# Kernel tuning notes

Measured on AMD Instinct MI355X. Metric: run time of the kernel, lower is better.

## Reference

```python
import jax, jax.numpy as jnp
import numpy as np

N = 40000   # nodes
E = 320000  # edges (avg degree 8)
H = 32      # hidden_dim
V = 128     # in_dim_node (node feature vocab)
EPS = 1e-5  # BatchNorm eps


def setup_inputs() -> dict:
    key = jax.random.key(0)
    ks = jax.random.split(key, 14)
    s = 0.05
    return {
        "h": jax.random.normal(ks[0], (N, H), jnp.float32),
        "e": jax.random.normal(ks[1], (E, H), jnp.float32),  # unused by forward (overwritten), kept for signature fidelity
        "feat": jax.random.randint(ks[2], (N,), 0, V),
        "src_idx": jax.random.randint(ks[3], (E,), 0, N),
        "dst_idx": jax.random.randint(ks[4], (E,), 0, N),
        "emb_src": jax.random.normal(ks[5], (V, H), jnp.float32) * s,
        "emb_dst": jax.random.normal(ks[6], (V, H), jnp.float32) * s,
        "W_edge": jax.random.normal(ks[7], (2 * H, H), jnp.float32) * s,
        "b_edge": jnp.zeros((H,), jnp.float32),
        "W1": jax.random.normal(ks[8], (H, H * H), jnp.float32) * s,  # proj1: H -> H^2
        "b1": jnp.zeros((H * H,), jnp.float32),
        "W2": jax.random.normal(ks[9], (H, H), jnp.float32) * s,      # proj2: H -> H
        "b2": jnp.zeros((H,), jnp.float32),
        "W3": jax.random.normal(ks[10], (H, H), jnp.float32) * s,     # edge_proj3
        "b3": jnp.zeros((H,), jnp.float32),
        "gamma": jnp.ones((H,), jnp.float32),
        "beta": jnp.zeros((H,), jnp.float32),
    }


def reference(h, e, feat, src_idx, dst_idx, emb_src, emb_dst, W_edge, b_edge,
              W1, b1, W2, b2, W3, b3, gamma, beta):
    # local edge term: embeddings of the integer node features at edge endpoints
    src = emb_src[feat[src_idx]]                      # [E, H]
    dst = emb_dst[feat[dst_idx]]                      # [E, H]
    lr_e_local = jnp.concatenate([src, dst], axis=-1) @ W_edge + b_edge  # [E, H]

    # global low-rank bilinear term. Original builds a dense [N, N, H] tensor
    # (mm of [N*H, H] with [H, N]) and gathers E rows; mathematically
    # out[e, k] = proj1(h[src_e]).reshape(H, H)[k, :] . proj2(h[dst_e]).
    # We compute only the E needed per-edge matvecs.
    P1 = (h @ W1 + b1).reshape(N, H, H)               # [N, H, H]
    P2 = h @ W2 + b2                                  # [N, H]
    lr_e_global = jnp.einsum('ekd,ed->ek', P1[src_idx], P2[dst_idx])  # [E, H]
    lr_e_global = lr_e_global @ W3 + b3

    out = lr_e_local + lr_e_global                    # [E, H]

    # BatchNorm1d over the edge batch (training-mode batch statistics, biased var)
    mean = jnp.mean(out, axis=0)
    var = jnp.mean(jnp.square(out - mean), axis=0)
    out = (out - mean) * jax.lax.rsqrt(var + EPS) * gamma + beta

    # ReLU; dropout omitted (deterministic eval-mode reference)
    return jax.nn.relu(out)
```

## Files before the change

kernel.cpp:

```cpp
#include <hip/hip_runtime.h>

#define N_NODES 40000
#define N_EDGES 320000
#define EPSBN 1e-5f

typedef float floatx4 __attribute__((ext_vector_type(4)));

__global__ void k_setup(const float* __restrict__ W1, float* __restrict__ w1t) {
  int i = blockIdx.x * 256 + threadIdx.x;
  int col = i >> 5, j = i & 31;
  w1t[col * 32 + j] = W1[j * 1024 + col];
}

__global__ void k_p2(const float* __restrict__ h, const float* __restrict__ W2,
                     const float* __restrict__ b2, float* __restrict__ P2) {
  __shared__ float w2s[1024];
  int t = threadIdx.x;
  for (int i = t; i < 1024; i += 256) w2s[i] = W2[i];
  __syncthreads();
  int nl = t >> 5, m = t & 31;
  int n = blockIdx.x * 8 + nl;
  const float* hrow = h + n * 32;
  float a = b2[m];
  #pragma unroll
  for (int j = 0; j < 32; ++j) a = fmaf(hrow[j], w2s[j * 32 + m], a);
  P2[n * 32 + m] = a;
}

__global__ __launch_bounds__(256) void k_edge(
    const float* __restrict__ h, const int* __restrict__ feat,
    const int* __restrict__ src_idx, const int* __restrict__ dst_idx,
    const float* __restrict__ emb_src, const float* __restrict__ emb_dst,
    const float* __restrict__ W_edge, const float* __restrict__ b_edge,
    const float* __restrict__ b1, const float* __restrict__ W3,
    const float* __restrict__ b3, const float* __restrict__ w1t,
    const float* __restrict__ P2, float* __restrict__ out,
    float* __restrict__ bn_acc) {
  __shared__ float red[4][64];
  const int t = threadIdx.x;
  const int e = blockIdx.x * 256 + t;
  const int si = src_idx[e], di = dst_idx[e];
  const int fs = feat[si], fd = feat[di];

  float p2r[32];
  #pragma unroll
  for (int d = 0; d < 32; ++d) p2r[d] = P2[di * 32 + d];

  float vout[32];
  #pragma unroll
  for (int m = 0; m < 32; ++m) vout[m] = b_edge[m] + b3[m];

  #pragma unroll
  for (int j = 0; j < 32; ++j) {
    float ej = emb_src[fs * 32 + j];
    #pragma unroll
    for (int m = 0; m < 32; ++m) vout[m] = fmaf(ej, W_edge[j * 32 + m], vout[m]);
  }
  #pragma unroll
  for (int j = 0; j < 32; ++j) {
    float ej = emb_dst[fd * 32 + j];
    #pragma unroll
    for (int m = 0; m < 32; ++m) vout[m] = fmaf(ej, W_edge[(32 + j) * 32 + m], vout[m]);
  }

  float hs[32];
  #pragma unroll
  for (int j = 0; j < 32; ++j) hs[j] = h[si * 32 + j];

  for (int k = 0; k < 32; ++k) {
    float gk = 0.f;
    #pragma unroll
    for (int d = 0; d < 32; ++d) {
      const float* w1c = w1t + (k * 32 + d) * 32;
      float tmp = b1[k * 32 + d];
      #pragma unroll
      for (int j = 0; j < 32; ++j) tmp = fmaf(hs[j], w1c[j], tmp);
      gk = fmaf(tmp, p2r[d], gk);
    }
    #pragma unroll
    for (int m = 0; m < 32; ++m) vout[m] = fmaf(gk, W3[k * 32 + m], vout[m]);
  }

  #pragma unroll
  for (int m = 0; m < 32; ++m) out[e * 32 + m] = vout[m];

  const int lane = t & 63, wv = t >> 6;
  #pragma unroll
  for (int m = 0; m < 32; ++m) {
    float a = vout[m];
    float b = vout[m] * vout[m];
    #pragma unroll
    for (int off = 1; off < 64; off <<= 1) {
      a += __shfl_xor(a, off);
      b += __shfl_xor(b, off);
    }
    if (lane == 0) { red[wv][m] = a; red[wv][32 + m] = b; }
  }
  __syncthreads();
  if (t < 64) {
    float acc = red[0][t] + red[1][t] + red[2][t] + red[3][t];
    atomicAdd(&bn_acc[t], acc);
  }
}

__global__ void k_bnfin(const float* __restrict__ bn, const float* __restrict__ gamma,
                        const float* __restrict__ beta, float* __restrict__ osc) {
  int m = threadIdx.x;
  float mean = bn[m] / (float)N_EDGES;
  float var = fmaxf(bn[32 + m] / (float)N_EDGES - mean * mean, 0.f);
  float sc = gamma[m] * rsqrtf(var + EPSBN);
  osc[m] = sc;
  osc[32 + m] = beta[m] - mean * sc;
}

__global__ void k_norm(float* __restrict__ out, const float* __restrict__ sc) {
  __shared__ float s[64];
  if (threadIdx.x < 64) s[threadIdx.x] = sc[threadIdx.x];
  __syncthreads();
  const int total = N_EDGES * 32 / 4;
  for (int i = blockIdx.x * blockDim.x + threadIdx.x; i < total; i += gridDim.x * blockDim.x) {
    floatx4 v = ((floatx4*)out)[i];
    int mb = (i * 4) & 31;
    floatx4 r;
    #pragma unroll
    for (int cc = 0; cc < 4; ++cc)
      r[cc] = fmaxf(fmaf(v[cc], s[mb + cc], s[32 + mb + cc]), 0.f);
    ((floatx4*)out)[i] = r;
  }
}

extern "C" void kernel_launch(void* const* d_in, const int* in_sizes, int n_in,
                              void* d_out, int out_size, void* d_ws, size_t ws_size,
                              hipStream_t stream) {
  const float* h       = (const float*)d_in[0];
  const int*   feat    = (const int*)d_in[2];
  const int*   srci    = (const int*)d_in[3];
  const int*   dsti    = (const int*)d_in[4];
  const float* emb_src = (const float*)d_in[5];
  const float* emb_dst = (const float*)d_in[6];
  const float* W_edge  = (const float*)d_in[7];
  const float* b_edge  = (const float*)d_in[8];
  const float* W1      = (const float*)d_in[9];
  const float* b1      = (const float*)d_in[10];
  const float* W2      = (const float*)d_in[11];
  const float* b2      = (const float*)d_in[12];
  const float* W3      = (const float*)d_in[13];
  const float* b3      = (const float*)d_in[14];
  const float* gamma   = (const float*)d_in[15];
  const float* beta    = (const float*)d_in[16];
  float* out = (float*)d_out;
  char* ws = (char*)d_ws;

  float* bn   = (float*)(ws + 0);
  float* osc  = (float*)(ws + 256);
  float* w1t  = (float*)(ws + 512);
  float* P2   = (float*)(ws + 512 + 131072);
  if (ws_size < (size_t)(512 + 131072 + 5120000)) return;

  hipMemsetAsync(bn, 0, 256, stream);
  k_setup<<<128, 256, 0, stream>>>(W1, w1t);
  k_p2<<<N_NODES / 8, 256, 0, stream>>>(h, W2, b2, P2);
  k_edge<<<N_EDGES / 256, 256, 0, stream>>>(h, feat, srci, dsti, emb_src, emb_dst,
                                            W_edge, b_edge, b1, W3, b3, w1t, P2, out, bn);
  k_bnfin<<<1, 32, 0, stream>>>(bn, gamma, beta, osc);
  k_norm<<<2048, 256, 0, stream>>>(out, osc);
}
```

Measured before the change: 877.8 us.

## Use fp16 MFMA for per-edge bilinear term and precompute embedding tables

The per-edge W1 projection of h[src] now runs on 16x16x32 fp16 MFMA with W1 and W3 staged in shared memory, in a persistent grid that handles 128 edges per iteration. The local edge term is folded into per-vocab lookup tables (Tsrc, Tdst), and the b1 bias contribution is folded into a per-node P2c precomputed alongside P2. Together these remove most of the scalar FMA work and the repeated weight reads from global memory per edge. The cost is fp16 rounding of h, W1 and W3, plus an extra N×H workspace buffer.

```diff
diff --git a/kernel.cpp b/kernel.cpp
--- a/kernel.cpp
+++ b/kernel.cpp
@@ -5,18 +5,67 @@
 #define EPSBN 1e-5f
 
 typedef float floatx4 __attribute__((ext_vector_type(4)));
-
-__global__ void k_setup(const float* __restrict__ W1, float* __restrict__ w1t) {
-  int i = blockIdx.x * 256 + threadIdx.x;
-  int col = i >> 5, j = i & 31;
-  w1t[col * 32 + j] = W1[j * 1024 + col];
+typedef _Float16 f16x8 __attribute__((ext_vector_type(8)));
+
+__device__ inline floatx4 mfma16(f16x8 a, f16x8 b, floatx4 c) {
+  return __builtin_amdgcn_mfma_f32_16x16x32_f16(a, b, c, 0, 0, 0);
+}
+
+__device__ inline f16x8 cvt8(floatx4 a, floatx4 b) {
+  f16x8 r;
+  r[0]=(_Float16)a[0]; r[1]=(_Float16)a[1]; r[2]=(_Float16)a[2]; r[3]=(_Float16)a[3];
+  r[4]=(_Float16)b[0]; r[5]=(_Float16)b[1]; r[6]=(_Float16)b[2]; r[7]=(_Float16)b[3];
+  return r;
+}
+
+__global__ void k_pre(const float* __restrict__ W1, const float* __restrict__ b1,
+                      const float* __restrict__ W3, const float* __restrict__ W_edge,
+                      const float* __restrict__ b_edge, const float* __restrict__ b3,
+                      const float* __restrict__ emb_src, const float* __restrict__ emb_dst,
+                      unsigned short* __restrict__ w1t, float* __restrict__ Tsrc,
+                      float* __restrict__ Tdst, unsigned short* __restrict__ w3h,
+                      float* __restrict__ BB) {
+  int t = threadIdx.x, bid = blockIdx.x;
+  if (bid < 128) {
+    int i = bid * 256 + t;
+    int q = i >> 5, j = i & 31;
+    w1t[i] = (unsigned short)__builtin_bit_cast(unsigned short, (_Float16)W1[j * 1024 + q]);
+  } else if (bid < 144) {
+    int i = (bid - 128) * 256 + t;
+    int v = i >> 5, m = i & 31;
+    float a = b_edge[m] + b3[m];
+    #pragma unroll
+    for (int j = 0; j < 32; ++j) a = fmaf(emb_src[v * 32 + j], W_edge[j * 32 + m], a);
+    Tsrc[i] = a;
+  } else if (bid < 160) {
+    int i = (bid - 144) * 256 + t;
+    int v = i >> 5, m = i & 31;
+    float a = 0.f;
+    #pragma unroll
+    for (int j = 0; j < 32; ++j) a = fmaf(emb_dst[v * 32 + j], W_edge[(32 + j) * 32 + m], a);
+    Tdst[i] = a;
+  } else if (bid == 160) {
+    #pragma unroll
+    for (int i = 0; i < 4; ++i) {
+      int idx = t * 4 + i;
+      w3h[idx] = (unsigned short)__builtin_bit_cast(unsigned short, (_Float16)W3[idx]);
+    }
+  } else {
+    int i = (bid - 161) * 256 + t;
+    int d = i >> 5, m = i & 31;
+    float a = 0.f;
+    #pragma unroll
+    for (int k = 0; k < 32; ++k) a = fmaf(b1[k * 32 + d], W3[k * 32 + m], a);
+    BB[i] = a;
+  }
 }
 
 __global__ void k_p2(const float* __restrict__ h, const float* __restrict__ W2,
-                     const float* __restrict__ b2, float* __restrict__ P2) {
-  __shared__ float w2s[1024];
+                     const float* __restrict__ b2, const float* __restrict__ BB,
+                     float* __restrict__ P2, float* __restrict__ P2c) {
+  __shared__ float w2s[1024], bbs[1024], p2l[8][32];
   int t = threadIdx.x;
-  for (int i = t; i < 1024; i += 256) w2s[i] = W2[i];
+  for (int i = t; i < 1024; i += 256) { w2s[i] = W2[i]; bbs[i] = BB[i]; }
   __syncthreads();
   int nl = t >> 5, m = t & 31;
   int n = blockIdx.x * 8 + nl;
@@ -25,80 +74,110 @@
   #pragma unroll
   for (int j = 0; j < 32; ++j) a = fmaf(hrow[j], w2s[j * 32 + m], a);
   P2[n * 32 + m] = a;
-}
-
-__global__ __launch_bounds__(256) void k_edge(
+  p2l[nl][m] = a;
+  __syncthreads();
+  float cacc = 0.f;
+  #pragma unroll
+  for (int d = 0; d < 32; ++d) cacc = fmaf(p2l[nl][d], bbs[d * 32 + m], cacc);
+  P2c[n * 32 + m] = cacc;
+}
+
+__global__ __launch_bounds__(512, 4) void k_edge(
     const float* __restrict__ h, const int* __restrict__ feat,
     const int* __restrict__ src_idx, const int* __restrict__ dst_idx,
-    const float* __restrict__ emb_src, const float* __restrict__ emb_dst,
-    const float* __restrict__ W_edge, const float* __restrict__ b_edge,
-    const float* __restrict__ b1, const float* __restrict__ W3,
-    const float* __restrict__ b3, const float* __restrict__ w1t,
-    const float* __restrict__ P2, float* __restrict__ out,
-    float* __restrict__ bn_acc) {
-  __shared__ float red[4][64];
+    const unsigned short* __restrict__ w1t, const unsigned short* __restrict__ w3h,
+    const float* __restrict__ Tsrc, const float* __restrict__ Tdst,
+    const float* __restrict__ P2, const float* __restrict__ P2c,
+    float* __restrict__ out, float* __restrict__ bn_acc) {
+  __shared__ unsigned short w1l[32768];
+  __shared__ unsigned short w3l[1024];
+  __shared__ float red[8][64];
   const int t = threadIdx.x;
-  const int e = blockIdx.x * 256 + t;
-  const int si = src_idx[e], di = dst_idx[e];
-  const int fs = feat[si], fd = feat[di];
-
-  float p2r[32];
+  for (int i = t; i < 4096; i += 512)
+    ((floatx4*)w1l)[i] = ((const floatx4*)w1t)[i];
+  if (t < 128) ((floatx4*)w3l)[t] = ((const floatx4*)w3h)[t];
+
+  const int lane = t & 63;
+  const int wv = t >> 6;
+  const int c = lane & 15;
+  const int g4 = lane >> 4;
+
+  float s8[8] = {0,0,0,0,0,0,0,0}, q8[8] = {0,0,0,0,0,0,0,0};
+
+  __syncthreads();
+
+  const unsigned short* awp = w1l + c * 32 + g4 * 8;
+  const unsigned short* w3p = w3l + g4 * 8;
+
+  for (int grp = blockIdx.x; grp < N_EDGES / 128; grp += gridDim.x) {
+    const int e = grp * 128 + wv * 16 + c;
+    const int si = src_idx[e];
+    const int di = dst_idx[e];
+    const int fs = feat[si];
+    const int fd = feat[di];
+
+    const floatx4* hp = (const floatx4*)(h + si * 32 + g4 * 8);
+    f16x8 bh = cvt8(hp[0], hp[1]);
+    const floatx4* pp = (const floatx4*)(P2 + di * 32);
+    floatx4 p2a = pp[g4];
+    floatx4 p2b = pp[g4 + 4];
+
+    float v8[8] = {0,0,0,0,0,0,0,0};
+    #pragma unroll
+    for (int k = 0; k < 32; ++k) {
+      f16x8 aw0 = *(const f16x8*)(awp + k * 1024);
+      f16x8 aw1 = *(const f16x8*)(awp + k * 1024 + 512);
+      floatx4 z = {0.f, 0.f, 0.f, 0.f};
+      floatx4 m0 = mfma16(aw0, bh, z);
+      floatx4 m1 = mfma16(aw1, bh, z);
+      float ps = m0[0] * p2a[0];
+      ps = fmaf(m0[1], p2a[1], ps);
+      ps = fmaf(m0[2], p2a[2], ps);
+      ps = fmaf(m0[3], p2a[3], ps);
+      ps = fmaf(m1[0], p2b[0], ps);
+      ps = fmaf(m1[1], p2b[1], ps);
+      ps = fmaf(m1[2], p2b[2], ps);
+      ps = fmaf(m1[3], p2b[3], ps);
+      ps += __shfl_xor(ps, 16);
+      ps += __shfl_xor(ps, 32);
+      const f16x8 w3k = *(const f16x8*)(w3p + k * 32);
+      #pragma unroll
+      for (int i = 0; i < 8; ++i) v8[i] = fmaf(ps, (float)w3k[i], v8[i]);
+    }
+
+    const floatx4* tsp = (const floatx4*)(Tsrc + fs * 32 + g4 * 8);
+    const floatx4* tdp = (const floatx4*)(Tdst + fd * 32 + g4 * 8);
+    const floatx4* pcp = (const floatx4*)(P2c + di * 32 + g4 * 8);
+    floatx4 o0, o1;
+    #pragma unroll
+    for (int i = 0; i < 4; ++i) {
+      o0[i] = v8[i] + tsp[0][i] + tdp[0][i] + pcp[0][i];
+      o1[i] = v8[4 + i] + tsp[1][i] + tdp[1][i] + pcp[1][i];
+    }
+    *(floatx4*)(out + e * 32 + g4 * 8) = o0;
+    *(floatx4*)(out + e * 32 + g4 * 8 + 4) = o1;
+    #pragma unroll
+    for (int i = 0; i < 4; ++i) {
+      s8[i] += o0[i];     q8[i] = fmaf(o0[i], o0[i], q8[i]);
+      s8[4 + i] += o1[i]; q8[4 + i] = fmaf(o1[i], o1[i], q8[4 + i]);
+    }
+  }
+
   #pragma unroll
-  for (int d = 0; d < 32; ++d) p2r[d] = P2[di * 32 + d];
-
-  float vout[32];
-  #pragma unroll
-  for (int m = 0; m < 32; ++m) vout[m] = b_edge[m] + b3[m];
-
-  #pragma unroll
-  for (int j = 0; j < 32; ++j) {
-    float ej = emb_src[fs * 32 + j];
-    #pragma unroll
-    for (int m = 0; m < 32; ++m) vout[m] = fmaf(ej, W_edge[j * 32 + m], vout[m]);
-  }
-  #pragma unroll
-  for (int j = 0; j < 32; ++j) {
-    float ej = emb_dst[fd * 32 + j];
-    #pragma unroll
-    for (int m = 0; m < 32; ++m) vout[m] = fmaf(ej, W_edge[(32 + j) * 32 + m], vout[m]);
-  }
-
-  float hs[32];
-  #pragma unroll
-  for (int j = 0; j < 32; ++j) hs[j] = h[si * 32 + j];
-
-  for (int k = 0; k < 32; ++k) {
-    float gk = 0.f;
-    #pragma unroll
-    for (int d = 0; d < 32; ++d) {
-      const float* w1c = w1t + (k * 32 + d) * 32;
-      float tmp = b1[k * 32 + d];
-      #pragma unroll
-      for (int j = 0; j < 32; ++j) tmp = fmaf(hs[j], w1c[j], tmp);
-      gk = fmaf(tmp, p2r[d], gk);
-    }
-    #pragma unroll
-    for (int m = 0; m < 32; ++m) vout[m] = fmaf(gk, W3[k * 32 + m], vout[m]);
-  }
-
-  #pragma unroll
-  for (int m = 0; m < 32; ++m) out[e * 32 + m] = vout[m];
-
-  const int lane = t & 63, wv = t >> 6;
-  #pragma unroll
-  for (int m = 0; m < 32; ++m) {
-    float a = vout[m];
-    float b = vout[m] * vout[m];
-    #pragma unroll
-    for (int off = 1; off < 64; off <<= 1) {
+  for (int i = 0; i < 8; ++i) {
+    float a = s8[i], b = q8[i];
+    #pragma unroll
+    for (int off = 1; off < 16; off <<= 1) {
       a += __shfl_xor(a, off);
       b += __shfl_xor(b, off);
     }
-    if (lane == 0) { red[wv][m] = a; red[wv][32 + m] = b; }
+    if (c == 0) { red[wv][g4 * 8 + i] = a; red[wv][32 + g4 * 8 + i] = b; }
   }
   __syncthreads();
   if (t < 64) {
-    float acc = red[0][t] + red[1][t] + red[2][t] + red[3][t];
+    float acc = 0.f;
+    #pragma unroll
+    for (int w = 0; w < 8; ++w) acc += red[w][t];
     atomicAdd(&bn_acc[t], acc);
   }
 }
@@ -151,17 +230,23 @@
   float* out = (float*)d_out;
   char* ws = (char*)d_ws;
 
-  float* bn   = (float*)(ws + 0);
-  float* osc  = (float*)(ws + 256);
-  float* w1t  = (float*)(ws + 512);
-  float* P2   = (float*)(ws + 512 + 131072);
-  if (ws_size < (size_t)(512 + 131072 + 5120000)) return;
+  float* bn            = (float*)(ws + 0);
+  float* osc           = (float*)(ws + 256);
+  float* Tsrc          = (float*)(ws + 512);
+  float* Tdst          = (float*)(ws + 512 + 16384);
+  float* BB            = (float*)(ws + 512 + 32768);
+  unsigned short* w3h  = (unsigned short*)(ws + 512 + 36864);
+  unsigned short* w1t  = (unsigned short*)(ws + 40960);
+  float* P2            = (float*)(ws + 106496);
+  float* P2c           = (float*)(ws + 106496 + 5120000);
+  if (ws_size < (size_t)(106496 + 2 * 5120000)) return;
 
   hipMemsetAsync(bn, 0, 256, stream);
-  k_setup<<<128, 256, 0, stream>>>(W1, w1t);
-  k_p2<<<N_NODES / 8, 256, 0, stream>>>(h, W2, b2, P2);
-  k_edge<<<N_EDGES / 256, 256, 0, stream>>>(h, feat, srci, dsti, emb_src, emb_dst,
-                                            W_edge, b_edge, b1, W3, b3, w1t, P2, out, bn);
+  k_pre<<<165, 256, 0, stream>>>(W1, b1, W3, W_edge, b_edge, b3, emb_src, emb_dst,
+                                 w1t, Tsrc, Tdst, w3h, BB);
+  k_p2<<<N_NODES / 8, 256, 0, stream>>>(h, W2, b2, BB, P2, P2c);
+  k_edge<<<512, 512, 0, stream>>>(h, feat, srci, dsti, w1t, w3h, Tsrc, Tdst,
+                                  P2, P2c, out, bn);
   k_bnfin<<<1, 32, 0, stream>>>(bn, gamma, beta, osc);
   k_norm<<<2048, 256, 0, stream>>>(out, osc);
 }
```

New measurement: 841.9 us. 4.1% less time.
